# Kernel optimization log

Hardware: AMD Instinct MI355X
Metric: run time of the kernel (lower is better)

Reference implementation:

```python
import jax, jax.numpy as jnp
import numpy as np

BS = 4
D = 256
N3 = BS * 80 * 80   # 25600 level-3 nodes
N4 = BS * 40 * 40   # 6400  level-4 nodes
N5 = BS * 20 * 20   # 1600  level-5 nodes
N = N3 + N4 + N5    # 33600 total graph nodes
EC = 260000         # contextual-graph edges (~8-neighborhood lattice)
EH = 120000         # hierarchical-graph edges (cross-scale)


def setup_inputs() -> dict:
    key = jax.random.key(0)
    ks = jax.random.split(key, 16)
    f = lambda k, s: jax.random.normal(k, s, dtype=jnp.float32) * 0.05
    return {
        # backbone features (yolov8-l channel widths)
        'c3': f(ks[0], (BS, 256, 80, 80)),
        'c4': f(ks[1], (BS, 512, 40, 40)),
        'c5': f(ks[2], (BS, 512, 20, 20)),
        # lateral 1x1 convs (stored as [out, in] since kernel is 1x1)
        'w3_1x1': f(ks[3], (256, 256)), 'b3_1x1': jnp.zeros((256,), jnp.float32),
        'w4_1x1': f(ks[4], (256, 512)), 'b4_1x1': jnp.zeros((256,), jnp.float32),
        'w5_1x1': f(ks[5], (256, 512)), 'b5_1x1': jnp.zeros((256,), jnp.float32),
        # output 3x3 convs
        'w3_3x3': f(ks[6], (256, 256, 3, 3)), 'b3_3x3': jnp.zeros((256,), jnp.float32),
        'w4_3x3': f(ks[7], (256, 256, 3, 3)), 'b4_3x3': jnp.zeros((256,), jnp.float32),
        'w5_3x3': f(ks[8], (256, 256, 3, 3)), 'b5_3x3': jnp.zeros((256,), jnp.float32),
        # 6 contextual + 3 hierarchical GNN layers (stacked)
        'Wc': f(ks[9], (6, 256, 256)), 'bc': jnp.zeros((6, 256), jnp.float32),
        'Wh': f(ks[10], (3, 256, 256)), 'bh': jnp.zeros((3, 256), jnp.float32),
        # edge lists (src -> dst message direction)
        'src_c': jax.random.randint(ks[11], (EC,), 0, N, dtype=jnp.int32),
        'dst_c': jax.random.randint(ks[12], (EC,), 0, N, dtype=jnp.int32),
        'src_h': jax.random.randint(ks[13], (EH,), 0, N, dtype=jnp.int32),
        'dst_h': jax.random.randint(ks[14], (EH,), 0, N, dtype=jnp.int32),
    }


def _conv1x1(x, w, b):
    return jnp.einsum('bchw,oc->bohw', x, w) + b[None, :, None, None]


def _conv3x3(x, w, b):
    y = jax.lax.conv_general_dilated(x, w, (1, 1), 'SAME')
    return y + b[None, :, None, None]


def _up2(x):
    return jnp.repeat(jnp.repeat(x, 2, axis=2), 2, axis=3)


def _degree(dst):
    d = jax.ops.segment_sum(jnp.ones(dst.shape, jnp.float32), dst, num_segments=N)
    return jnp.maximum(d, 1.0)[:, None]


def _gnn_layer(h, W, b, src, dst, deg):
    # gather-aggregate-scatter: mean over incoming messages + self, then linear+relu
    agg = jax.ops.segment_sum(h[src], dst, num_segments=N) / deg  # [N, D]
    return jax.nn.relu((h + agg) @ W + b)


def reference(c3, c4, c5,
              w3_1x1, b3_1x1, w4_1x1, b4_1x1, w5_1x1, b5_1x1,
              w3_3x3, b3_3x3, w4_3x3, b4_3x3, w5_3x3, b5_3x3,
              Wc, bc, Wh, bh,
              src_c, dst_c, src_h, dst_h):
    p3 = _conv1x1(c3, w3_1x1, b3_1x1)  # [BS,256,80,80]
    p4 = _conv1x1(c4, w4_1x1, b4_1x1)  # [BS,256,40,40]
    p5 = _conv1x1(c5, w5_1x1, b5_1x1)  # [BS,256,20,20]

    # CNN -> graph node features (NHWC flatten, cat levels)
    h = jnp.concatenate([
        p3.transpose(0, 2, 3, 1).reshape(-1, D),
        p4.transpose(0, 2, 3, 1).reshape(-1, D),
        p5.transpose(0, 2, 3, 1).reshape(-1, D),
    ], axis=0)  # [N, 256]

    deg_c = _degree(dst_c)
    deg_h = _degree(dst_h)
    for i in range(3):                       # context1..3
        h = _gnn_layer(h, Wc[i], bc[i], src_c, dst_c, deg_c)
    for i in range(3):                       # hierarch1..3
        h = _gnn_layer(h, Wh[i], bh[i], src_h, dst_h, deg_h)
    for i in range(3, 6):                    # context4..6
        h = _gnn_layer(h, Wc[i], bc[i], src_c, dst_c, deg_c)

    # graph -> CNN
    p3g = h[:N3].reshape(BS, 80, 80, D).transpose(0, 3, 1, 2)
    p4g = h[N3:N3 + N4].reshape(BS, 40, 40, D).transpose(0, 3, 1, 2)
    p5g = h[N3 + N4:].reshape(BS, 20, 20, D).transpose(0, 3, 1, 2)

    p5 = p5 + p5g
    p4 = p4 + _up2(p5) + p4g
    p3 = p3 + _up2(p4) + p3g

    out3 = _conv3x3(p3, w3_3x3, b3_3x3)
    out4 = _conv3x3(p4, w4_3x3, b4_3x3)
    out5 = _conv3x3(p5, w5_3x3, b5_3x3)
    return out3, out4, out5
```

## Files before the change

### kernel.cpp

```cpp
#include <hip/hip_runtime.h>
#include <stdint.h>

#define N3i 25600
#define N4i 6400
#define N5i 1600
#define NNi 33600
#define ECi 260000
#define EHi 120000

typedef unsigned short u16;
typedef __bf16 bf16x8 __attribute__((ext_vector_type(8)));
typedef float f32x4 __attribute__((ext_vector_type(4)));
typedef unsigned short u16x8 __attribute__((ext_vector_type(8)));

__device__ __forceinline__ float b2f(u16 u) {
    union { float f; uint32_t i; } v; v.i = ((uint32_t)u) << 16; return v.f;
}
__device__ __forceinline__ u16 f2b(float f) {
    union { float f; uint32_t i; } v; v.f = f;
    uint32_t x = v.i;
    uint32_t r = (x + 0x7FFFu + ((x >> 16) & 1u)) >> 16;
    return (u16)r;
}

__device__ __forceinline__ void gll16(const u16* g, u16* l) {
    __builtin_amdgcn_global_load_lds((const __attribute__((address_space(1))) void*)g,
                                     (__attribute__((address_space(3))) void*)l, 16, 0, 0);
}

__global__ void detect_kernel(const void* __restrict__ c3raw, int* __restrict__ flag,
                              uint32_t* __restrict__ zp) {
    const uint32_t* p = (const uint32_t*)c3raw;
    int t = threadIdx.x;
    zp[t] = 0;
    int vote = 0;
    for (int i = t; i < 256; i += 64) {
        uint32_t w = p[i];
        uint32_t lo = w & 0xFFFFu;
        uint32_t e = (lo >> 7) & 0xFFu;
        if (lo == 0u || (e >= 100u && e <= 127u)) vote++;
    }
#pragma unroll
    for (int d = 32; d >= 1; d >>= 1) vote += __shfl_down(vote, d, 64);
    if (t == 0) flag[0] = (vote >= 192) ? 1 : 0;
}

__global__ void zero_i32(int* p, int n) {
    int i = blockIdx.x * 256 + threadIdx.x;
    if (i < n) p[i] = 0;
}

__global__ void hist2_kernel(const int* __restrict__ dst_c, const int* __restrict__ dst_h,
                             int* __restrict__ cnt_c, int* __restrict__ cnt_h) {
    int i = blockIdx.x * 256 + threadIdx.x;
    if (i < ECi) {
        int d = dst_c[i];
        if ((unsigned)d < (unsigned)NNi) atomicAdd(&cnt_c[d], 1);
    } else {
        int j = i - ECi;
        if (j < EHi) {
            int d = dst_h[j];
            if ((unsigned)d < (unsigned)NNi) atomicAdd(&cnt_h[d], 1);
        }
    }
}

__global__ __launch_bounds__(1024) void scan2_kernel(
    const int* __restrict__ cnt_c, int* __restrict__ rs_c, int* __restrict__ cur_c,
    float* __restrict__ inv_c,
    const int* __restrict__ cnt_h, int* __restrict__ rs_h, int* __restrict__ cur_h,
    float* __restrict__ inv_h, int n) {
    const int* cnt = blockIdx.x ? cnt_h : cnt_c;
    int* rs = blockIdx.x ? rs_h : rs_c;
    int* cur = blockIdx.x ? cur_h : cur_c;
    float* inv = blockIdx.x ? inv_h : inv_c;
    __shared__ int ws[16];
    __shared__ int base;
    int t = threadIdx.x, wid = t >> 6, lane = t & 63;
    if (t == 0) { base = 0; rs[0] = 0; }
    __syncthreads();
    for (int i0 = 0; i0 < n; i0 += 1024) {
        int i = i0 + t;
        int v = (i < n) ? cnt[i] : 0;
        int x = v;
#pragma unroll
        for (int d = 1; d < 64; d <<= 1) {
            int y = __shfl_up(x, d, 64);
            if (lane >= d) x += y;
        }
        if (lane == 63) ws[wid] = x;
        __syncthreads();
        if (wid == 0) {
            int s = (lane < 16) ? ws[lane] : 0;
#pragma unroll
            for (int d = 1; d < 16; d <<= 1) {
                int y = __shfl_up(s, d, 64);
                if (lane >= d) s += y;
            }
            if (lane < 16) ws[lane] = s;
        }
        __syncthreads();
        int b = base;
        int incl = x + (wid ? ws[wid - 1] : 0);
        if (i < n) {
            rs[i + 1] = b + incl;
            cur[i] = b + incl - v;
            int dv = v < 1 ? 1 : v;
            inv[i] = 1.0f / (float)dv;
        }
        int tot = ws[15];
        __syncthreads();
        if (t == 1023) base = b + tot;
        __syncthreads();
    }
}

__global__ void fill2_kernel(const int* __restrict__ src_c, const int* __restrict__ dst_c,
                             int* __restrict__ cur_c, int* __restrict__ csr_c,
                             const int* __restrict__ src_h, const int* __restrict__ dst_h,
                             int* __restrict__ cur_h, int* __restrict__ csr_h) {
    int i = blockIdx.x * 256 + threadIdx.x;
    if (i < ECi) {
        int d = dst_c[i];
        if ((unsigned)d < (unsigned)NNi) {
            int p = atomicAdd(&cur_c[d], 1);
            if ((unsigned)p < (unsigned)ECi) csr_c[p] = src_c[i];
        }
    } else {
        int j = i - ECi;
        if (j < EHi) {
            int d = dst_h[j];
            if ((unsigned)d < (unsigned)NNi) {
                int p = atomicAdd(&cur_h[d], 1);
                if ((unsigned)p < (unsigned)EHi) csr_h[p] = src_h[j];
            }
        }
    }
}

struct CvtJobs { const void* src[11]; u16* dst[11]; int n[11]; };

__global__ void cvt_all_kernel(CvtJobs j, const int* __restrict__ flag) {
    int job = blockIdx.y;
    int i = blockIdx.x * 256 + threadIdx.x;
    if (i >= j.n[job]) return;
    const void* s = j.src[job];
    j.dst[job][i] = flag[0] ? ((const u16*)s)[i] : f2b(((const float*)s)[i]);
}

__device__ __forceinline__ void tin_body(const void* in, size_t ioff, u16* outp, int R, int C,
                                         int isb, int c0, int r0, u16 (*tile)[33]) {
    const u16* inb = (const u16*)in + ioff;
    const float* inf_ = (const float*)in + ioff;
    int tx = threadIdx.x, ty = threadIdx.y;
#pragma unroll
    for (int i = 0; i < 4; i++) {
        int r = r0 + ty + i * 8, c = c0 + tx;
        if (r < R && c < C) {
            size_t idx = (size_t)r * C + c;
            tile[ty + i * 8][tx] = isb ? inb[idx] : f2b(inf_[idx]);
        }
    }
    __syncthreads();
#pragma unroll
    for (int i = 0; i < 4; i++) {
        int c = c0 + ty + i * 8, r = r0 + tx;
        if (c < C && r < R) outp[(size_t)c * R + r] = tile[tx][ty + i * 8];
    }
}

__global__ void transpose_in3(const void* __restrict__ c3, const void* __restrict__ c4,
                              const void* __restrict__ c5, u16* __restrict__ Xt3,
                              u16* __restrict__ Xt4, u16* __restrict__ Xt5,
                              const int* __restrict__ flag) {
    __shared__ u16 tile[32][33];
    int bx = blockIdx.x;
    const void* in; u16* outb; int R, C, xb;
    if (bx < 200)      { in = c3; outb = Xt3; R = 256; C = 6400; xb = bx; }
    else if (bx < 250) { in = c4; outb = Xt4; R = 512; C = 1600; xb = bx - 200; }
    else               { in = c5; outb = Xt5; R = 512; C = 400;  xb = bx - 250; }
    int r0 = blockIdx.y * 32;
    if (r0 >= R) return;
    size_t boff = (size_t)blockIdx.z * R * C;
    tin_body(in, boff, outb + boff, R, C, flag[0], xb * 32, r0, tile);
}

__global__ void transpose_w(const void* __restrict__ Wc, const void* __restrict__ Wh,
                            u16* __restrict__ WtG, const int* __restrict__ flag) {
    __shared__ u16 tile[32][33];
    int z = blockIdx.z;
    const void* in = (z < 6) ? Wc : Wh;
    int zi = (z < 6) ? z : z - 6;
    tin_body(in, (size_t)zi * 65536, WtG + (size_t)z * 65536, 256, 256, flag[0],
             blockIdx.x * 32, blockIdx.y * 32, tile);
}

__global__ void transpose_out3(const u16* __restrict__ OutT, void* __restrict__ outv,
                               const int* __restrict__ flag) {
    __shared__ u16 tile[32][33];
    int by = blockIdx.y;
    const u16* inb; size_t out_off; int R, yb;
    if (by < 200)      { inb = OutT; out_off = 0; R = 6400; yb = by; }
    else if (by < 250) { inb = OutT + (size_t)N3i * 256; out_off = (size_t)4 * 256 * 6400; R = 1600; yb = by - 200; }
    else               { inb = OutT + (size_t)(N3i + N4i) * 256; out_off = (size_t)4 * 256 * 8000; R = 400; yb = by - 250; }
    int r0 = yb * 32;
    if (r0 >= R) return;
    const int C = 256;
    int isb = flag[0];
    int c0 = blockIdx.x * 32;
    size_t boff = (size_t)blockIdx.z * R * C;
    const u16* inp = inb + boff;
    int tx = threadIdx.x, ty = threadIdx.y;
#pragma unroll
    for (int i = 0; i < 4; i++) {
        int r = r0 + ty + i * 8, c = c0 + tx;
        if (r < R && c < C) tile[ty + i * 8][tx] = inp[(size_t)r * C + c];
    }
    __syncthreads();
#pragma unroll
    for (int i = 0; i < 4; i++) {
        int c = c0 + ty + i * 8, r = r0 + tx;
        if (c < C && r < R) {
            size_t o = out_off + boff + (size_t)c * R + r;
            u16 v = tile[tx][ty + i * 8];
            if (isb) ((u16*)outv)[o] = v;
            else ((float*)outv)[o] = b2f(v);
        }
    }
}

__global__ void convw3_kernel(const void* __restrict__ w0, const void* __restrict__ w1,
                              const void* __restrict__ w2, u16* __restrict__ WtC,
                              const int* __restrict__ flag) {
    int lvl = blockIdx.y;
    const void* w = (lvl == 0) ? w0 : (lvl == 1) ? w1 : w2;
    u16* wt = WtC + (size_t)lvl * 256 * 2304;
    int i = blockIdx.x * 256 + threadIdx.x;
    if (i >= 256 * 2304) return;
    int n = i / 2304;
    int k = i - n * 2304;
    int tap = k >> 8, ci = k & 255;
    int si = n * 2304 + ci * 9 + tap;
    wt[i] = flag[0] ? ((const u16*)w)[si] : f2b(((const float*)w)[si]);
}

__global__ __launch_bounds__(256) void gather_kernel(
    const u16* __restrict__ H, const int* __restrict__ csr, const int* __restrict__ rs,
    const float* __restrict__ invdeg, u16* __restrict__ T, int ecap) {
    int node = blockIdx.x * 4 + (threadIdx.x >> 6);
    if (node >= NNi) return;
    int lane = threadIdx.x & 63;
    int half = lane >> 5;
    int c = (lane & 31) * 8;
    int e0 = rs[node], e1 = rs[node + 1];
    e0 = e0 < 0 ? 0 : e0;
    e1 = e1 > ecap ? ecap : e1;
    const u16* Hn = H + (size_t)node * 256 + c;
    u16x8 self = *(const u16x8*)Hn;
    float s0 = 0.f, s1 = 0.f, s2 = 0.f, s3 = 0.f, s4 = 0.f, s5 = 0.f, s6 = 0.f, s7 = 0.f;
    int e = e0 + half;
    int srcn = (e < e1) ? csr[e] : 0;
    for (; e < e1; e += 2) {
        int src = srcn;
        if (e + 2 < e1) srcn = csr[e + 2];
        src = ((unsigned)src < (unsigned)NNi) ? src : 0;
        u16x8 hv = *(const u16x8*)(H + (size_t)src * 256 + c);
        s0 += b2f(hv[0]); s1 += b2f(hv[1]); s2 += b2f(hv[2]); s3 += b2f(hv[3]);
        s4 += b2f(hv[4]); s5 += b2f(hv[5]); s6 += b2f(hv[6]); s7 += b2f(hv[7]);
    }
    s0 += __shfl_xor(s0, 32, 64); s1 += __shfl_xor(s1, 32, 64);
    s2 += __shfl_xor(s2, 32, 64); s3 += __shfl_xor(s3, 32, 64);
    s4 += __shfl_xor(s4, 32, 64); s5 += __shfl_xor(s5, 32, 64);
    s6 += __shfl_xor(s6, 32, 64); s7 += __shfl_xor(s7, 32, 64);
    if (half == 0) {
        float inv = invdeg[node];
        u16x8 o;
        o[0] = f2b(b2f(self[0]) + s0 * inv); o[1] = f2b(b2f(self[1]) + s1 * inv);
        o[2] = f2b(b2f(self[2]) + s2 * inv); o[3] = f2b(b2f(self[3]) + s3 * inv);
        o[4] = f2b(b2f(self[4]) + s4 * inv); o[5] = f2b(b2f(self[5]) + s5 * inv);
        o[6] = f2b(b2f(self[6]) + s6 * inv); o[7] = f2b(b2f(self[7]) + s7 * inv);
        *(u16x8*)(T + (size_t)node * 256 + c) = o;
    }
}

template <bool CONV, bool RELU>
__device__ __forceinline__ void gemm_body(
    u16 (* __restrict__ lds)[4096],
    const u16* __restrict__ A, int lda,
    const u16* __restrict__ Bt, int ldb,
    const u16* __restrict__ bias,
    const u16* __restrict__ zp,
    u16* __restrict__ out, u16* __restrict__ out2,
    int M, int K, int H, int W, int m0, int n0) {
    int t = threadIdx.x;
    int w = t >> 6, lane = t & 63;
    int wm = w & 1, wn = w >> 1;
    f32x4 acc[4][4] = {};

    int g0 = w * 128 + lane;
    int g1 = g0 + 64;
    int row0 = g0 >> 2, c0 = g0 & 3;
    int row1 = g1 >> 2, c1 = g1 & 3;
    int ss0 = ((c0 ^ ((row0 >> 1) & 3)) << 3);
    int ss1 = ((c1 ^ ((row1 >> 1) & 3)) << 3);

    int ar0 = m0 + row0, ar1 = m0 + row1;
    bool aok0 = ar0 < M, aok1 = ar1 < M;
    int y0_ = 0, x0_ = 0, y1_ = 0, x1_ = 0;
    if (CONV) {
        int HW = H * W;
        if (aok0) { int b = ar0 / HW; int rem = ar0 - b * HW; y0_ = rem / W; x0_ = rem - y0_ * W; }
        if (aok1) { int b = ar1 / HW; int rem = ar1 - b * HW; y1_ = rem / W; x1_ = rem - y1_ * W; }
    }
    const u16* aP0 = A + (size_t)ar0 * lda + ss0;
    const u16* aP1 = A + (size_t)ar1 * lda + ss1;
    const u16* bP0 = Bt + (size_t)(n0 + row0) * ldb + ss0;
    const u16* bP1 = Bt + (size_t)(n0 + row1) * ldb + ss1;

    int lbase = w * 1024;

    auto stage = [&](int bf, int k0) {
        u16* LA = lds[bf * 2];
        u16* LB = lds[bf * 2 + 1];
        const u16* sa0;
        const u16* sa1;
        if (!CONV) {
            sa0 = aok0 ? aP0 + k0 : zp;
            sa1 = aok1 ? aP1 + k0 : zp;
        } else {
            int tap = k0 >> 8;
            int t3 = tap / 3;
            int dy = t3 - 1, dx = tap - t3 * 3 - 1;
            int off = (dy * W + dx) * lda + (k0 & 255);
            int yy0 = y0_ + dy, xx0 = x0_ + dx;
            int yy1 = y1_ + dy, xx1 = x1_ + dx;
            sa0 = (aok0 && (unsigned)yy0 < (unsigned)H && (unsigned)xx0 < (unsigned)W) ? aP0 + off : zp;
            sa1 = (aok1 && (unsigned)yy1 < (unsigned)H && (unsigned)xx1 < (unsigned)W) ? aP1 + off : zp;
        }
        gll16(sa0, LA + lbase);
        gll16(sa1, LA + lbase + 512);
        gll16(bP0 + k0, LB + lbase);
        gll16(bP1 + k0, LB + lbase + 512);
    };

    int nst = K >> 5;
    int fm = lane & 15;
    int co = (((lane >> 4) ^ ((fm >> 1) & 3)) << 3);

    stage(0, 0);
    __syncthreads();
    for (int s = 0; s < nst; s++) {
        int bf = s & 1;
        if (s + 1 < nst) stage(bf ^ 1, (s + 1) << 5);
        const u16* LA = lds[bf * 2];
        const u16* LB = lds[bf * 2 + 1];
        bf16x8 af[4], bfv[4];
#pragma unroll
        for (int i = 0; i < 4; i++) af[i] = *(const bf16x8*)&LA[(wm * 64 + i * 16 + fm) * 32 + co];
#pragma unroll
        for (int j = 0; j < 4; j++) bfv[j] = *(const bf16x8*)&LB[(wn * 64 + j * 16 + fm) * 32 + co];
#pragma unroll
        for (int i = 0; i < 4; i++)
#pragma unroll
            for (int j = 0; j < 4; j++)
                acc[i][j] = __builtin_amdgcn_mfma_f32_16x16x32_bf16(af[i], bfv[j], acc[i][j], 0, 0, 0);
        __syncthreads();
    }

    int q = lane >> 4, nl = lane & 15;
#pragma unroll
    for (int j = 0; j < 4; j++) {
        int n = n0 + wn * 64 + j * 16 + nl;
        float bv = b2f(bias[n]);
#pragma unroll
        for (int i = 0; i < 4; i++) {
            int mbase = m0 + wm * 64 + i * 16 + q * 4;
#pragma unroll
            for (int rg = 0; rg < 4; rg++) {
                int m = mbase + rg;
                if (m < M) {
                    float v = acc[i][j][rg] + bv;
                    if (RELU) v = fmaxf(v, 0.f);
                    u16 bs = f2b(v);
                    out[(size_t)m * 256 + n] = bs;
                    if (out2) out2[(size_t)m * 256 + n] = bs;
                }
            }
        }
    }
}

template <bool CONV, bool RELU>
__global__ __launch_bounds__(256) void gemm_kernel(
    const u16* __restrict__ A, int lda,
    const u16* __restrict__ Bt, int ldb,
    const u16* __restrict__ bias,
    const u16* __restrict__ zp,
    u16* __restrict__ out, u16* __restrict__ out2,
    int M, int K, int H, int W) {
    __shared__ __align__(16) u16 lds[4][4096];
    gemm_body<CONV, RELU>(lds, A, lda, Bt, ldb, bias, zp, out, out2, M, K, H, W,
                          blockIdx.y * 128, blockIdx.x * 128);
}

__global__ __launch_bounds__(256) void lat_all_kernel(
    const u16* __restrict__ Xt3, const u16* __restrict__ Xt4, const u16* __restrict__ Xt5,
    const u16* __restrict__ W1, const u16* __restrict__ BB, const u16* __restrict__ zp,
    u16* __restrict__ P, u16* __restrict__ Ha) {
    __shared__ __align__(16) u16 lds[4][4096];
    int by = blockIdx.y;
    const u16* A; const u16* Bt; const u16* bias;
    int K, Ml, m0; size_t off;
    if (by < 200)      { A = Xt3; Bt = W1;          bias = BB;       K = 256; Ml = N3i; off = 0;                          m0 = by * 128; }
    else if (by < 250) { A = Xt4; Bt = W1 + 65536;  bias = BB + 256; K = 512; Ml = N4i; off = (size_t)N3i * 256;          m0 = (by - 200) * 128; }
    else               { A = Xt5; Bt = W1 + 196608; bias = BB + 512; K = 512; Ml = N5i; off = (size_t)(N3i + N4i) * 256;  m0 = (by - 250) * 128; }
    gemm_body<false, false>(lds, A, K, Bt, K, bias, zp, P + off, Ha + off, Ml, K, 0, 0,
                            m0, blockIdx.x * 128);
}

__global__ __launch_bounds__(256) void conv_gemm_all(
    const u16* __restrict__ Pc, const u16* __restrict__ WtC,
    const u16* __restrict__ BB, const u16* __restrict__ zp, u16* __restrict__ OutT) {
    __shared__ __align__(16) u16 lds[4][4096];
    int by = blockIdx.y;
    int lvl, yl, Hd, Ml; size_t base;
    if (by < 200)      { lvl = 0; yl = by;       Hd = 80; Ml = N3i; base = 0; }
    else if (by < 250) { lvl = 1; yl = by - 200; Hd = 40; Ml = N4i; base = (size_t)N3i * 256; }
    else               { lvl = 2; yl = by - 250; Hd = 20; Ml = N5i; base = (size_t)(N3i + N4i) * 256; }
    gemm_body<true, false>(lds, Pc + base, 256, WtC + (size_t)lvl * 256 * 2304, 2304,
                           BB + 3072 + lvl * 256, zp, OutT + base, nullptr,
                           Ml, 2304, Hd, Hd, yl * 128, blockIdx.x * 128);
}

__global__ void pyr_kernel(const u16* __restrict__ P, const u16* __restrict__ Hf,
                           u16* __restrict__ Pc) {
    int i = blockIdx.x * 256 + threadIdx.x;
    if (i >= NNi * 64) return;
    int node = i >> 6, c = (i & 63) * 4;
    size_t bi = (size_t)node * 256 + c;
    ushort4 pv = *(const ushort4*)(P + bi);
    ushort4 hv = *(const ushort4*)(Hf + bi);
    float v0 = b2f(pv.x) + b2f(hv.x);
    float v1 = b2f(pv.y) + b2f(hv.y);
    float v2 = b2f(pv.z) + b2f(hv.z);
    float v3 = b2f(pv.w) + b2f(hv.w);
    if (node < N3i) {
        int b = node / 6400, rem = node - b * 6400;
        int y = rem / 80, x = rem - y * 80;
        size_t s4 = ((size_t)N3i + b * 1600 + (y >> 1) * 40 + (x >> 1)) * 256 + c;
        size_t s5 = ((size_t)(N3i + N4i) + b * 400 + (y >> 2) * 20 + (x >> 2)) * 256 + c;
        ushort4 p4 = *(const ushort4*)(P + s4), h4 = *(const ushort4*)(Hf + s4);
        ushort4 p5 = *(const ushort4*)(P + s5), h5 = *(const ushort4*)(Hf + s5);
        v0 += b2f(p4.x) + b2f(h4.x) + b2f(p5.x) + b2f(h5.x);
        v1 += b2f(p4.y) + b2f(h4.y) + b2f(p5.y) + b2f(h5.y);
        v2 += b2f(p4.z) + b2f(h4.z) + b2f(p5.z) + b2f(h5.z);
        v3 += b2f(p4.w) + b2f(h4.w) + b2f(p5.w) + b2f(h5.w);
    } else if (node < N3i + N4i) {
        int n4 = node - N3i;
        int b = n4 / 1600, rem = n4 - b * 1600;
        int y = rem / 40, x = rem - y * 40;
        size_t s5 = ((size_t)(N3i + N4i) + b * 400 + (y >> 1) * 20 + (x >> 1)) * 256 + c;
        ushort4 p5 = *(const ushort4*)(P + s5), h5 = *(const ushort4*)(Hf + s5);
        v0 += b2f(p5.x) + b2f(h5.x);
        v1 += b2f(p5.y) + b2f(h5.y);
        v2 += b2f(p5.z) + b2f(h5.z);
        v3 += b2f(p5.w) + b2f(h5.w);
    }
    ushort4 o;
    o.x = f2b(v0); o.y = f2b(v1); o.z = f2b(v2); o.w = f2b(v3);
    *(ushort4*)(Pc + bi) = o;
}

extern "C" void kernel_launch(void* const* d_in, const int* in_sizes, int n_in,
                              void* d_out, int out_size, void* d_ws, size_t ws_size,
                              hipStream_t stream) {
    (void)in_sizes; (void)n_in; (void)out_size; (void)ws_size;
    const void* c3 = d_in[0];
    const void* c4 = d_in[1];
    const void* c5 = d_in[2];
    const void* w3_1 = d_in[3];
    const void* b3_1 = d_in[4];
    const void* w4_1 = d_in[5];
    const void* b4_1 = d_in[6];
    const void* w5_1 = d_in[7];
    const void* b5_1 = d_in[8];
    const void* w3_3 = d_in[9];
    const void* b3_3 = d_in[10];
    const void* w4_3 = d_in[11];
    const void* b4_3 = d_in[12];
    const void* w5_3 = d_in[13];
    const void* b5_3 = d_in[14];
    const void* Wc = d_in[15];
    const void* bc = d_in[16];
    const void* Wh = d_in[17];
    const void* bh = d_in[18];
    const int* src_c = (const int*)d_in[19];
    const int* dst_c = (const int*)d_in[20];
    const int* src_h = (const int*)d_in[21];
    const int* dst_h = (const int*)d_in[22];

    char* w = (char*)d_ws;
    auto alloc = [&](size_t bytes) -> void* {
        void* p = (void*)w;
        w += (bytes + 255) & ~(size_t)255;
        return p;
    };
    u16* XT  = (u16*)alloc(((size_t)N3i * 256 + (size_t)N4i * 512 + (size_t)N5i * 512) * 2);
    u16* Xt3 = XT;
    u16* Xt4 = XT + (size_t)N3i * 256;
    u16* Xt5 = Xt4 + (size_t)N4i * 512;
    u16* T   = XT;
    u16* Pc  = XT;
    u16* WtC = XT + (size_t)NNi * 256;
    u16* WtG = (u16*)alloc((size_t)9 * 65536 * 2);
    u16* W1  = (u16*)alloc((size_t)(65536 + 131072 + 131072) * 2);
    u16* BB  = (u16*)alloc((size_t)3840 * 2);
    u16* P   = (u16*)alloc((size_t)NNi * 256 * 2);
    u16* Ha  = (u16*)alloc((size_t)NNi * 256 * 2);
    u16* Hb  = (u16*)d_out;
    int* csr_c = (int*)alloc((size_t)ECi * 4);
    int* csr_h = (int*)alloc((size_t)EHi * 4);
    int* cnt2  = (int*)alloc((size_t)2 * NNi * 4);
    int* cnt_c = cnt2;
    int* cnt_h = cnt2 + NNi;
    int* rs_c  = (int*)alloc((size_t)(NNi + 1) * 4);
    int* rs_h  = (int*)alloc((size_t)(NNi + 1) * 4);
    int* cur_c = (int*)alloc((size_t)NNi * 4);
    int* cur_h = (int*)alloc((size_t)NNi * 4);
    float* inv_c = (float*)alloc((size_t)NNi * 4);
    float* inv_h = (float*)alloc((size_t)NNi * 4);
    int* flag  = (int*)alloc(256);
    u16* zp    = (u16*)alloc(256);

    detect_kernel<<<1, 64, 0, stream>>>(c3, flag, (uint32_t*)zp);

    zero_i32<<<(2 * NNi + 255) / 256, 256, 0, stream>>>(cnt2, 2 * NNi);
    hist2_kernel<<<(ECi + EHi + 255) / 256, 256, 0, stream>>>(dst_c, dst_h, cnt_c, cnt_h);
    scan2_kernel<<<2, 1024, 0, stream>>>(cnt_c, rs_c, cur_c, inv_c,
                                         cnt_h, rs_h, cur_h, inv_h, NNi);
    fill2_kernel<<<(ECi + EHi + 255) / 256, 256, 0, stream>>>(
        src_c, dst_c, cur_c, csr_c, src_h, dst_h, cur_h, csr_h);

    CvtJobs cj;
    cj.src[0] = w3_1; cj.dst[0] = W1;          cj.n[0] = 65536;
    cj.src[1] = w4_1; cj.dst[1] = W1 + 65536;  cj.n[1] = 131072;
    cj.src[2] = w5_1; cj.dst[2] = W1 + 196608; cj.n[2] = 131072;
    cj.src[3] = b3_1; cj.dst[3] = BB;          cj.n[3] = 256;
    cj.src[4] = b4_1; cj.dst[4] = BB + 256;    cj.n[4] = 256;
    cj.src[5] = b5_1; cj.dst[5] = BB + 512;    cj.n[5] = 256;
    cj.src[6] = bc;   cj.dst[6] = BB + 768;    cj.n[6] = 1536;
    cj.src[7] = bh;   cj.dst[7] = BB + 2304;   cj.n[7] = 768;
    cj.src[8] = b3_3; cj.dst[8] = BB + 3072;   cj.n[8] = 256;
    cj.src[9] = b4_3; cj.dst[9] = BB + 3328;   cj.n[9] = 256;
    cj.src[10] = b5_3; cj.dst[10] = BB + 3584; cj.n[10] = 256;
    cvt_all_kernel<<<dim3(512, 11), 256, 0, stream>>>(cj, flag);

    transpose_in3<<<dim3(263, 16, 4), dim3(32, 8), 0, stream>>>(c3, c4, c5, Xt3, Xt4, Xt5, flag);
    transpose_w<<<dim3(8, 8, 9), dim3(32, 8), 0, stream>>>(Wc, Wh, WtG, flag);

    lat_all_kernel<<<dim3(2, 263), 256, 0, stream>>>(Xt3, Xt4, Xt5, W1, BB, zp, P, Ha);

    convw3_kernel<<<dim3(2304, 3), 256, 0, stream>>>(w3_3, w4_3, w5_3, WtC, flag);

    u16* Hcur = Ha;
    u16* Hnxt = Hb;
    for (int l = 0; l < 9; l++) {
        bool ctx = (l < 3) || (l >= 6);
        const int* csr = ctx ? csr_c : csr_h;
        const int* rs = ctx ? rs_c : rs_h;
        const float* inv = ctx ? inv_c : inv_h;
        int ecap = ctx ? ECi : EHi;
        int wi = (l < 3) ? l : (l < 6 ? 6 + (l - 3) : l - 3);
        const u16* bias = (l < 3) ? BB + 768 + l * 256
                        : (l < 6 ? BB + 2304 + (l - 3) * 256 : BB + 768 + (l - 3) * 256);
        gather_kernel<<<(NNi + 3) / 4, 256, 0, stream>>>(Hcur, csr, rs, inv, T, ecap);
        gemm_kernel<false, true><<<dim3(2, 263), 256, 0, stream>>>(
            T, 256, WtG + (size_t)wi * 65536, 256, bias, zp, Hnxt, nullptr, NNi, 256, 0, 0);
        u16* tmp = Hcur; Hcur = Hnxt; Hnxt = tmp;
    }
    u16* OutT = Hnxt;

    pyr_kernel<<<(NNi * 64 + 255) / 256, 256, 0, stream>>>(P, Hcur, Pc);

    conv_gemm_all<<<dim3(2, 263), 256, 0, stream>>>(Pc, WtC, BB, zp, OutT);

    transpose_out3<<<dim3(8, 263, 4), dim3(32, 8), 0, stream>>>(OutT, d_out, flag);
}
```

Measured before the change: 686.7 us.

## Triple-buffer GEMM LDS pipeline with vmcnt waits and unroll gather loop

The shared GEMM body moves from double to triple buffering in LDS. It issues loads two stages ahead, waits with an explicit s_waitcnt vmcnt plus a single barrier per step, and raises wave priority around the MFMA block. The goal is to hide global-to-LDS latency and drop one barrier per iteration, at the cost of 48KB of LDS per block, which may lower occupancy. The gather kernel is also unrolled to two independent edge loads per iteration with separate accumulators, which raises memory-level parallelism.

```diff
diff --git a/kernel.cpp b/kernel.cpp
--- a/kernel.cpp
+++ b/kernel.cpp
@@ -257,28 +257,41 @@
     e1 = e1 > ecap ? ecap : e1;
     const u16* Hn = H + (size_t)node * 256 + c;
     u16x8 self = *(const u16x8*)Hn;
-    float s0 = 0.f, s1 = 0.f, s2 = 0.f, s3 = 0.f, s4 = 0.f, s5 = 0.f, s6 = 0.f, s7 = 0.f;
+    float a0 = 0.f, a1 = 0.f, a2 = 0.f, a3 = 0.f, a4 = 0.f, a5 = 0.f, a6 = 0.f, a7 = 0.f;
+    float b0 = 0.f, b1 = 0.f, b2 = 0.f, b3 = 0.f, b4 = 0.f, b5 = 0.f, b6 = 0.f, b7 = 0.f;
     int e = e0 + half;
-    int srcn = (e < e1) ? csr[e] : 0;
-    for (; e < e1; e += 2) {
-        int src = srcn;
-        if (e + 2 < e1) srcn = csr[e + 2];
-        src = ((unsigned)src < (unsigned)NNi) ? src : 0;
-        u16x8 hv = *(const u16x8*)(H + (size_t)src * 256 + c);
-        s0 += b2f(hv[0]); s1 += b2f(hv[1]); s2 += b2f(hv[2]); s3 += b2f(hv[3]);
-        s4 += b2f(hv[4]); s5 += b2f(hv[5]); s6 += b2f(hv[6]); s7 += b2f(hv[7]);
-    }
-    s0 += __shfl_xor(s0, 32, 64); s1 += __shfl_xor(s1, 32, 64);
-    s2 += __shfl_xor(s2, 32, 64); s3 += __shfl_xor(s3, 32, 64);
-    s4 += __shfl_xor(s4, 32, 64); s5 += __shfl_xor(s5, 32, 64);
-    s6 += __shfl_xor(s6, 32, 64); s7 += __shfl_xor(s7, 32, 64);
+    while (e + 2 < e1) {
+        int i0 = csr[e];
+        int i1 = csr[e + 2];
+        i0 = ((unsigned)i0 < (unsigned)NNi) ? i0 : 0;
+        i1 = ((unsigned)i1 < (unsigned)NNi) ? i1 : 0;
+        u16x8 h0 = *(const u16x8*)(H + (size_t)i0 * 256 + c);
+        u16x8 h1 = *(const u16x8*)(H + (size_t)i1 * 256 + c);
+        a0 += b2f(h0[0]); a1 += b2f(h0[1]); a2 += b2f(h0[2]); a3 += b2f(h0[3]);
+        a4 += b2f(h0[4]); a5 += b2f(h0[5]); a6 += b2f(h0[6]); a7 += b2f(h0[7]);
+        b0 += b2f(h1[0]); b1 += b2f(h1[1]); b2 += b2f(h1[2]); b3 += b2f(h1[3]);
+        b4 += b2f(h1[4]); b5 += b2f(h1[5]); b6 += b2f(h1[6]); b7 += b2f(h1[7]);
+        e += 4;
+    }
+    if (e < e1) {
+        int i0 = csr[e];
+        i0 = ((unsigned)i0 < (unsigned)NNi) ? i0 : 0;
+        u16x8 h0 = *(const u16x8*)(H + (size_t)i0 * 256 + c);
+        a0 += b2f(h0[0]); a1 += b2f(h0[1]); a2 += b2f(h0[2]); a3 += b2f(h0[3]);
+        a4 += b2f(h0[4]); a5 += b2f(h0[5]); a6 += b2f(h0[6]); a7 += b2f(h0[7]);
+    }
+    a0 += b0; a1 += b1; a2 += b2; a3 += b3; a4 += b4; a5 += b5; a6 += b6; a7 += b7;
+    a0 += __shfl_xor(a0, 32, 64); a1 += __shfl_xor(a1, 32, 64);
+    a2 += __shfl_xor(a2, 32, 64); a3 += __shfl_xor(a3, 32, 64);
+    a4 += __shfl_xor(a4, 32, 64); a5 += __shfl_xor(a5, 32, 64);
+    a6 += __shfl_xor(a6, 32, 64); a7 += __shfl_xor(a7, 32, 64);
     if (half == 0) {
         float inv = invdeg[node];
         u16x8 o;
-        o[0] = f2b(b2f(self[0]) + s0 * inv); o[1] = f2b(b2f(self[1]) + s1 * inv);
-        o[2] = f2b(b2f(self[2]) + s2 * inv); o[3] = f2b(b2f(self[3]) + s3 * inv);
-        o[4] = f2b(b2f(self[4]) + s4 * inv); o[5] = f2b(b2f(self[5]) + s5 * inv);
-        o[6] = f2b(b2f(self[6]) + s6 * inv); o[7] = f2b(b2f(self[7]) + s7 * inv);
+        o[0] = f2b(b2f(self[0]) + a0 * inv); o[1] = f2b(b2f(self[1]) + a1 * inv);
+        o[2] = f2b(b2f(self[2]) + a2 * inv); o[3] = f2b(b2f(self[3]) + a3 * inv);
+        o[4] = f2b(b2f(self[4]) + a4 * inv); o[5] = f2b(b2f(self[5]) + a5 * inv);
+        o[6] = f2b(b2f(self[6]) + a6 * inv); o[7] = f2b(b2f(self[7]) + a7 * inv);
         *(u16x8*)(T + (size_t)node * 256 + c) = o;
     }
 }
@@ -319,7 +332,8 @@
 
     int lbase = w * 1024;
 
-    auto stage = [&](int bf, int k0) {
+    auto stage = [&](int bf, int ks) {
+        int k0 = ks << 5;
         u16* LA = lds[bf * 2];
         u16* LB = lds[bf * 2 + 1];
         const u16* sa0;
@@ -348,10 +362,16 @@
     int co = (((lane >> 4) ^ ((fm >> 1) & 3)) << 3);
 
     stage(0, 0);
-    __syncthreads();
+    stage(1, 1);
     for (int s = 0; s < nst; s++) {
-        int bf = s & 1;
-        if (s + 1 < nst) stage(bf ^ 1, (s + 1) << 5);
+        int bf = s % 3;
+        if (s + 1 < nst) {
+            asm volatile("s_waitcnt vmcnt(4)" ::: "memory");
+        } else {
+            asm volatile("s_waitcnt vmcnt(0)" ::: "memory");
+        }
+        __builtin_amdgcn_s_barrier();
+        if (s + 2 < nst) stage((s + 2) % 3, s + 2);
         const u16* LA = lds[bf * 2];
         const u16* LB = lds[bf * 2 + 1];
         bf16x8 af[4], bfv[4];
@@ -359,12 +379,13 @@
         for (int i = 0; i < 4; i++) af[i] = *(const bf16x8*)&LA[(wm * 64 + i * 16 + fm) * 32 + co];
 #pragma unroll
         for (int j = 0; j < 4; j++) bfv[j] = *(const bf16x8*)&LB[(wn * 64 + j * 16 + fm) * 32 + co];
+        __builtin_amdgcn_s_setprio(1);
 #pragma unroll
         for (int i = 0; i < 4; i++)
 #pragma unroll
             for (int j = 0; j < 4; j++)
                 acc[i][j] = __builtin_amdgcn_mfma_f32_16x16x32_bf16(af[i], bfv[j], acc[i][j], 0, 0, 0);
-        __syncthreads();
+        __builtin_amdgcn_s_setprio(0);
     }
 
     int q = lane >> 4, nl = lane & 15;
@@ -398,7 +419,7 @@
     const u16* __restrict__ zp,
     u16* __restrict__ out, u16* __restrict__ out2,
     int M, int K, int H, int W) {
-    __shared__ __align__(16) u16 lds[4][4096];
+    __shared__ __align__(16) u16 lds[6][4096];
     gemm_body<CONV, RELU>(lds, A, lda, Bt, ldb, bias, zp, out, out2, M, K, H, W,
                           blockIdx.y * 128, blockIdx.x * 128);
 }
@@ -407,7 +428,7 @@
     const u16* __restrict__ Xt3, const u16* __restrict__ Xt4, const u16* __restrict__ Xt5,
     const u16* __restrict__ W1, const u16* __restrict__ BB, const u16* __restrict__ zp,
     u16* __restrict__ P, u16* __restrict__ Ha) {
-    __shared__ __align__(16) u16 lds[4][4096];
+    __shared__ __align__(16) u16 lds[6][4096];
     int by = blockIdx.y;
     const u16* A; const u16* Bt; const u16* bias;
     int K, Ml, m0; size_t off;
@@ -421,7 +442,7 @@
 __global__ __launch_bounds__(256) void conv_gemm_all(
     const u16* __restrict__ Pc, const u16* __restrict__ WtC,
     const u16* __restrict__ BB, const u16* __restrict__ zp, u16* __restrict__ OutT) {
-    __shared__ __align__(16) u16 lds[4][4096];
+    __shared__ __align__(16) u16 lds[6][4096];
     int by = blockIdx.y;
     int lvl, yl, Hd, Ml; size_t base;
     if (by < 200)      { lvl = 0; yl = by;       Hd = 80; Ml = N3i; base = 0; }
```

After: 698.3 us. No clear change (+1.7%).

## Rework gather to one half-wave per node with shuffled batched index loads

Applied to the files above, without the earlier changes.

The neighbor-aggregation kernel now assigns 32 lanes per node instead of 64, so each block covers 8 nodes. Edge indices are loaded cooperatively, 32 at a time, and broadcast with shuffles, and four neighbor rows are fetched per iteration into two accumulator sets to raise memory-level parallelism. This removes the cross-half reduction and the serial per-edge index prefetch. In exchange it uses more registers and adds shuffle overhead. Nodes with few edges leave much of each 32-lane index load unused.

```diff
diff --git a/kernel.cpp b/kernel.cpp
--- a/kernel.cpp
+++ b/kernel.cpp
@@ -247,40 +247,67 @@
 __global__ __launch_bounds__(256) void gather_kernel(
     const u16* __restrict__ H, const int* __restrict__ csr, const int* __restrict__ rs,
     const float* __restrict__ invdeg, u16* __restrict__ T, int ecap) {
-    int node = blockIdx.x * 4 + (threadIdx.x >> 6);
+    int node = blockIdx.x * 8 + (threadIdx.x >> 5);
     if (node >= NNi) return;
-    int lane = threadIdx.x & 63;
-    int half = lane >> 5;
-    int c = (lane & 31) * 8;
+    int L = threadIdx.x & 31;
+    int c = L * 8;
     int e0 = rs[node], e1 = rs[node + 1];
     e0 = e0 < 0 ? 0 : e0;
     e1 = e1 > ecap ? ecap : e1;
-    const u16* Hn = H + (size_t)node * 256 + c;
-    u16x8 self = *(const u16x8*)Hn;
-    float s0 = 0.f, s1 = 0.f, s2 = 0.f, s3 = 0.f, s4 = 0.f, s5 = 0.f, s6 = 0.f, s7 = 0.f;
-    int e = e0 + half;
-    int srcn = (e < e1) ? csr[e] : 0;
-    for (; e < e1; e += 2) {
-        int src = srcn;
-        if (e + 2 < e1) srcn = csr[e + 2];
-        src = ((unsigned)src < (unsigned)NNi) ? src : 0;
-        u16x8 hv = *(const u16x8*)(H + (size_t)src * 256 + c);
-        s0 += b2f(hv[0]); s1 += b2f(hv[1]); s2 += b2f(hv[2]); s3 += b2f(hv[3]);
-        s4 += b2f(hv[4]); s5 += b2f(hv[5]); s6 += b2f(hv[6]); s7 += b2f(hv[7]);
-    }
-    s0 += __shfl_xor(s0, 32, 64); s1 += __shfl_xor(s1, 32, 64);
-    s2 += __shfl_xor(s2, 32, 64); s3 += __shfl_xor(s3, 32, 64);
-    s4 += __shfl_xor(s4, 32, 64); s5 += __shfl_xor(s5, 32, 64);
-    s6 += __shfl_xor(s6, 32, 64); s7 += __shfl_xor(s7, 32, 64);
-    if (half == 0) {
-        float inv = invdeg[node];
-        u16x8 o;
-        o[0] = f2b(b2f(self[0]) + s0 * inv); o[1] = f2b(b2f(self[1]) + s1 * inv);
-        o[2] = f2b(b2f(self[2]) + s2 * inv); o[3] = f2b(b2f(self[3]) + s3 * inv);
-        o[4] = f2b(b2f(self[4]) + s4 * inv); o[5] = f2b(b2f(self[5]) + s5 * inv);
-        o[6] = f2b(b2f(self[6]) + s6 * inv); o[7] = f2b(b2f(self[7]) + s7 * inv);
-        *(u16x8*)(T + (size_t)node * 256 + c) = o;
-    }
+    u16x8 self = *(const u16x8*)(H + (size_t)node * 256 + c);
+    float a0 = 0.f, a1 = 0.f, a2 = 0.f, a3 = 0.f, a4 = 0.f, a5 = 0.f, a6 = 0.f, a7 = 0.f;
+    float b0 = 0.f, b1 = 0.f, b2 = 0.f, b3 = 0.f, b4 = 0.f, b5 = 0.f, b6 = 0.f, b7 = 0.f;
+    for (int base = e0; base < e1; base += 32) {
+        int ee = base + L;
+        int iv = 0;
+        if (ee < e1) {
+            iv = csr[ee];
+            iv = ((unsigned)iv < (unsigned)NNi) ? iv : 0;
+        }
+        int cnt = e1 - base;
+        cnt = cnt > 32 ? 32 : cnt;
+        int k = 0;
+        for (; k + 3 < cnt; k += 4) {
+            int j0 = __shfl(iv, k, 32), j1 = __shfl(iv, k + 1, 32);
+            int j2 = __shfl(iv, k + 2, 32), j3 = __shfl(iv, k + 3, 32);
+            u16x8 h0 = *(const u16x8*)(H + (size_t)j0 * 256 + c);
+            u16x8 h1 = *(const u16x8*)(H + (size_t)j1 * 256 + c);
+            u16x8 h2 = *(const u16x8*)(H + (size_t)j2 * 256 + c);
+            u16x8 h3 = *(const u16x8*)(H + (size_t)j3 * 256 + c);
+            a0 += b2f(h0[0]); a1 += b2f(h0[1]); a2 += b2f(h0[2]); a3 += b2f(h0[3]);
+            a4 += b2f(h0[4]); a5 += b2f(h0[5]); a6 += b2f(h0[6]); a7 += b2f(h0[7]);
+            b0 += b2f(h1[0]); b1 += b2f(h1[1]); b2 += b2f(h1[2]); b3 += b2f(h1[3]);
+            b4 += b2f(h1[4]); b5 += b2f(h1[5]); b6 += b2f(h1[6]); b7 += b2f(h1[7]);
+            a0 += b2f(h2[0]); a1 += b2f(h2[1]); a2 += b2f(h2[2]); a3 += b2f(h2[3]);
+            a4 += b2f(h2[4]); a5 += b2f(h2[5]); a6 += b2f(h2[6]); a7 += b2f(h2[7]);
+            b0 += b2f(h3[0]); b1 += b2f(h3[1]); b2 += b2f(h3[2]); b3 += b2f(h3[3]);
+            b4 += b2f(h3[4]); b5 += b2f(h3[5]); b6 += b2f(h3[6]); b7 += b2f(h3[7]);
+        }
+        if (k + 1 < cnt) {
+            int j0 = __shfl(iv, k, 32), j1 = __shfl(iv, k + 1, 32);
+            u16x8 h0 = *(const u16x8*)(H + (size_t)j0 * 256 + c);
+            u16x8 h1 = *(const u16x8*)(H + (size_t)j1 * 256 + c);
+            a0 += b2f(h0[0]); a1 += b2f(h0[1]); a2 += b2f(h0[2]); a3 += b2f(h0[3]);
+            a4 += b2f(h0[4]); a5 += b2f(h0[5]); a6 += b2f(h0[6]); a7 += b2f(h0[7]);
+            b0 += b2f(h1[0]); b1 += b2f(h1[1]); b2 += b2f(h1[2]); b3 += b2f(h1[3]);
+            b4 += b2f(h1[4]); b5 += b2f(h1[5]); b6 += b2f(h1[6]); b7 += b2f(h1[7]);
+            k += 2;
+        }
+        if (k < cnt) {
+            int j0 = __shfl(iv, k, 32);
+            u16x8 h0 = *(const u16x8*)(H + (size_t)j0 * 256 + c);
+            a0 += b2f(h0[0]); a1 += b2f(h0[1]); a2 += b2f(h0[2]); a3 += b2f(h0[3]);
+            a4 += b2f(h0[4]); a5 += b2f(h0[5]); a6 += b2f(h0[6]); a7 += b2f(h0[7]);
+        }
+    }
+    a0 += b0; a1 += b1; a2 += b2; a3 += b3; a4 += b4; a5 += b5; a6 += b6; a7 += b7;
+    float inv = invdeg[node];
+    u16x8 o;
+    o[0] = f2b(b2f(self[0]) + a0 * inv); o[1] = f2b(b2f(self[1]) + a1 * inv);
+    o[2] = f2b(b2f(self[2]) + a2 * inv); o[3] = f2b(b2f(self[3]) + a3 * inv);
+    o[4] = f2b(b2f(self[4]) + a4 * inv); o[5] = f2b(b2f(self[5]) + a5 * inv);
+    o[6] = f2b(b2f(self[6]) + a6 * inv); o[7] = f2b(b2f(self[7]) + a7 * inv);
+    *(u16x8*)(T + (size_t)node * 256 + c) = o;
 }
 
 template <bool CONV, bool RELU>
@@ -573,7 +600,7 @@
         int wi = (l < 3) ? l : (l < 6 ? 6 + (l - 3) : l - 3);
         const u16* bias = (l < 3) ? BB + 768 + l * 256
                         : (l < 6 ? BB + 2304 + (l - 3) * 256 : BB + 768 + (l - 3) * 256);
-        gather_kernel<<<(NNi + 3) / 4, 256, 0, stream>>>(Hcur, csr, rs, inv, T, ecap);
+        gather_kernel<<<NNi / 8, 256, 0, stream>>>(Hcur, csr, rs, inv, T, ecap);
         gemm_kernel<false, true><<<dim3(2, 263), 256, 0, stream>>>(
             T, 256, WtG + (size_t)wi * 65536, 256, bias, zp, Hnxt, nullptr, NNi, 256, 0, 0);
         u16* tmp = Hcur; Hcur = Hnxt; Hnxt = tmp;
```

Result: faster. 670.4 us (-2.4%).
